# Kernel tuning notes

Hardware: AMD Instinct MI355X
Metric: run time of the kernel (lower is better)

Reference implementation:

```python
import jax, jax.numpy as jnp
import numpy as np
import math

B, S, D, H = 2, 2048, 2048, 16
DH = D // H  # head dim = 128
THETA = 10000.0


def _rope(x, pos):
    """Interleaved RoPE. x: [..., S, DH], pos: [S] (int)."""
    dh = x.shape[-1]
    freqs = (1.0 / THETA) ** (2.0 * jnp.arange(dh // 2, dtype=jnp.float32) / dh)  # [DH/2]
    ang = pos.astype(jnp.float32)[:, None] * freqs[None, :]  # [S, DH/2]
    cos = jnp.cos(ang).astype(x.dtype)
    sin = jnp.sin(ang).astype(x.dtype)
    xe = x[..., 0::2]
    xo = x[..., 1::2]
    oe = xe * cos - xo * sin
    oo = xe * sin + xo * cos
    return jnp.stack([oe, oo], axis=-1).reshape(x.shape)


def setup_inputs() -> dict:
    key = jax.random.key(0)
    ks = jax.random.split(key, 5)
    std = 2.0 / math.sqrt(D + D)
    x = jax.random.normal(ks[0], (B, S, D), dtype=jnp.float32)
    Wq = jax.random.normal(ks[1], (D, D), dtype=jnp.float32) * std
    Wk = jax.random.normal(ks[2], (D, D), dtype=jnp.float32) * std
    Wv = jax.random.normal(ks[3], (D, D), dtype=jnp.float32) * std
    Wo = jax.random.normal(ks[4], (D, D), dtype=jnp.float32) * std
    token_positions = jnp.arange(S, dtype=jnp.int64 if jax.config.jax_enable_x64 else jnp.int32)[None, :]
    return {"x": x, "token_positions": token_positions, "Wq": Wq, "Wk": Wk, "Wv": Wv, "Wo": Wo}


def reference(x, token_positions, Wq, Wk, Wv, Wo):
    b, s, d = x.shape
    pos = token_positions[0]  # [S]
    # QKV projections (Linear is x @ W.T, no bias)
    Q = (x @ Wq.T).reshape(b, s, H, DH).transpose(0, 2, 1, 3)  # [b,h,s,dh]
    K = (x @ Wk.T).reshape(b, s, H, DH).transpose(0, 2, 1, 3)
    V = (x @ Wv.T).reshape(b, s, H, DH).transpose(0, 2, 1, 3)
    # per-head RoPE on Q and K
    Q = _rope(Q, pos)
    K = _rope(K, pos)
    # scaled dot-product attention with causal mask
    scores = jnp.einsum('bhqd,bhkd->bhqk', Q, K) / math.sqrt(DH)
    causal = jnp.tril(jnp.ones((s, s), dtype=bool))  # [s,s]
    scores = jnp.where(causal[None, None, :, :], scores, -jnp.inf)
    prob = jax.nn.softmax(scores, axis=-1)
    O = jnp.einsum('bhqk,bhkd->bhqd', prob, V)  # [b,h,s,dh]
    O = O.transpose(0, 2, 1, 3).reshape(b, s, d)
    return O @ Wo.T
```

## Files before the change

kernel.cpp:

```cpp
#include <hip/hip_runtime.h>
#include <hip/hip_bf16.h>
#include <math.h>

#define BB 2
#define SS 2048
#define DD 2048
#define HH 16
#define DHH 128
#define MM (BB*SS)

typedef __attribute__((ext_vector_type(8))) short bf16x8;
typedef __attribute__((ext_vector_type(4))) float f32x4;

#define AS1 __attribute__((address_space(1)))
#define AS3 __attribute__((address_space(3)))
#define GLOAD_LDS16(g, l) __builtin_amdgcn_global_load_lds((const AS1 void*)(g), (AS3 void*)(l), 16, 0, 0)

#if __has_builtin(__builtin_amdgcn_exp2f)
#define EXP2F(x) __builtin_amdgcn_exp2f(x)
#else
#define EXP2F(x) exp2f(x)
#endif

__device__ __forceinline__ float b2f(short s) {
  union { unsigned int u; float f; } v;
  v.u = ((unsigned int)(unsigned short)s) << 16;
  return v.f;
}
__device__ __forceinline__ short f2b(float f) {
  union { float f; unsigned int u; } v; v.f = f;
  unsigned int u = v.u;
  u += 0x7fffu + ((u >> 16) & 1u);
  return (short)(u >> 16);
}
__device__ __forceinline__ short f2b_fast(float f) {
  union { float f; unsigned int u; } v; v.f = f;
  return (short)((v.u + 0x8000u) >> 16);
}

template<int CTRL>
__device__ __forceinline__ float dppf(float x) {
  int xi = __builtin_bit_cast(int, x);
  int r = __builtin_amdgcn_update_dpp(0, xi, CTRL, 0xf, 0xf, true);
  return __builtin_bit_cast(float, r);
}
__device__ __forceinline__ float rmax16(float x) {
  x = fmaxf(x, dppf<0xB1>(x));
  x = fmaxf(x, dppf<0x4E>(x));
  x = fmaxf(x, dppf<0x141>(x));
  x = fmaxf(x, dppf<0x140>(x));
  return x;
}
__device__ __forceinline__ float rsum16(float x) {
  x += dppf<0xB1>(x);
  x += dppf<0x4E>(x);
  x += dppf<0x141>(x);
  x += dppf<0x140>(x);
  return x;
}

__global__ void cvt_all(const float* __restrict__ x,  const float* __restrict__ wq,
                        const float* __restrict__ wk, const float* __restrict__ wv,
                        const float* __restrict__ wo,
                        short* __restrict__ xb,  short* __restrict__ wqb,
                        short* __restrict__ wkb, short* __restrict__ wvb,
                        short* __restrict__ wob) {
  int i = blockIdx.x * blockDim.x + threadIdx.x;
  const float* src; short* dst; int off;
  if (i < 2097152) { src = x; dst = xb; off = i; }
  else {
    int j = i - 2097152;
    int w = j >> 20; off = j & 1048575;
    src = (w == 0) ? wq : (w == 1) ? wk : (w == 2) ? wv : wo;
    dst = (w == 0) ? wqb : (w == 1) ? wkb : (w == 2) ? wvb : wob;
  }
  float4 v = ((const float4*)src)[i < 2097152 ? off : off];
  short4 o;
  o.x = f2b(v.x); o.y = f2b(v.y); o.z = f2b(v.z); o.w = f2b(v.w);
  ((short4*)dst)[off] = o;
}

#define LDA3(b, mt, kk) (*(const bf16x8*)((const char*)smA + (b)*32768 + \
    (wm*64 + (mt)*16 + l16)*128 + ((((kk)*64) + quad*16) ^ ((l16 & 7) << 4))))
#define LDB3(b, nt, kk) (*(const bf16x8*)((const char*)smB + (b)*16384 + \
    (wn*64 + (nt)*16 + l16)*128 + ((((kk)*64) + quad*16) ^ ((l16 & 7) << 4))))
#define STGA4(b, t) do { \
    _Pragma("unroll") \
    for (int h = 0; h < 4; ++h) \
      GLOAD_LDS16(aBase + (size_t)(h*64) * DD + (t)*64, smA + (b)*16384 + h*4096 + wst); } while(0)
#define STGB2M(b, t) do { \
    _Pragma("unroll") \
    for (int h = 0; h < 2; ++h) \
      GLOAD_LDS16(bBase + (size_t)(h*64) * DD + (t)*64, smB + (b)*8192 + h*4096 + wst); } while(0)
#define MFMA_P(NT0) do { \
    __builtin_amdgcn_s_setprio(1); \
    _Pragma("unroll") \
    for (int mt = 0; mt < 4; ++mt) \
      _Pragma("unroll") \
      for (int nt = 0; nt < 2; ++nt) \
        _Pragma("unroll") \
        for (int kk = 0; kk < 2; ++kk) \
          acc[mt][(NT0) + nt] = __builtin_amdgcn_mfma_f32_16x16x32_bf16( \
              af[mt][kk], bf[(NT0) + nt][kk], acc[mt][(NT0) + nt], 0, 0, 0); \
    __builtin_amdgcn_s_setprio(0); } while(0)

#define GEMM_KLOOP \
  STGA4(0, 0); STGB2M(0, 0); \
  STGA4(1, 1); STGB2M(1, 1); \
  asm volatile("s_waitcnt vmcnt(6)" ::: "memory"); \
  __builtin_amdgcn_s_barrier(); \
  int bc = 0, bs = 2; \
  for (int t = 0; t < 32; ++t) { \
    _Pragma("unroll") \
    for (int mt = 0; mt < 4; ++mt) { af[mt][0] = LDA3(bc, mt, 0); af[mt][1] = LDA3(bc, mt, 1); } \
    _Pragma("unroll") \
    for (int nt = 0; nt < 2; ++nt) { bf[nt][0] = LDB3(bc, nt, 0); bf[nt][1] = LDB3(bc, nt, 1); } \
    if (t + 2 < 32) STGA4(bs, t + 2); \
    __builtin_amdgcn_s_barrier(); \
    asm volatile("s_waitcnt lgkmcnt(0)" ::: "memory"); \
    __builtin_amdgcn_sched_barrier(0); \
    MFMA_P(0); \
    __builtin_amdgcn_s_barrier(); \
    _Pragma("unroll") \
    for (int nt = 2; nt < 4; ++nt) { bf[nt][0] = LDB3(bc, nt, 0); bf[nt][1] = LDB3(bc, nt, 1); } \
    if (t + 2 < 32) { \
      STGB2M(bs, t + 2); \
      asm volatile("s_waitcnt vmcnt(6)" ::: "memory"); \
    } else { \
      asm volatile("s_waitcnt vmcnt(0)" ::: "memory"); \
    } \
    __builtin_amdgcn_s_barrier(); \
    asm volatile("s_waitcnt lgkmcnt(0)" ::: "memory"); \
    __builtin_amdgcn_sched_barrier(0); \
    MFMA_P(2); \
    __builtin_amdgcn_s_barrier(); \
    bc = (bc == 2) ? 0 : bc + 1; \
    bs = (bs == 2) ? 0 : bs + 1; \
  }

__global__ __launch_bounds__(512, 1)
void gemm_qkv(const short* __restrict__ A,
              const short* __restrict__ Wq, const short* __restrict__ Wk,
              const short* __restrict__ Wv, const int* __restrict__ pos,
              short* __restrict__ Qo, short* __restrict__ Ko, short* __restrict__ Vo) {
  __shared__ __align__(16) short sm[73728];
  const int tid = threadIdx.x;
  const int lane = tid & 63;
  const int wave = tid >> 6;
  const int quad = lane >> 4, l16 = lane & 15;
  const int wm = wave >> 1, wn = wave & 1;

  const int wid = (blockIdx.x & 7) * 96 + (blockIdx.x >> 3);
  const int wsel = wid >> 8;
  const int idr = wid & 255;
  const int bm = (idr >> 4) * 256;
  const int bn = (idr & 15) * 128;
  const short* Bw = (wsel == 0) ? Wq : (wsel == 1) ? Wk : Wv;
  short* Cout = (wsel == 0) ? Qo : (wsel == 1) ? Ko : Vo;

  short* smA = sm;
  short* smB = sm + 49152;
  const int wst = wave * 512;

  const int srow = tid >> 3;
  const int scol = ((tid & 7) ^ (srow & 7)) * 8;
  const short* aBase = A  + (size_t)(bm + srow) * DD + scol;
  const short* bBase = Bw + (size_t)(bn + srow) * DD + scol;

  f32x4 acc[4][4] = {};
  bf16x8 af[4][2], bf[4][2];

  GEMM_KLOOP

  if (wsel < 2) {
    const float post = (wsel == 0) ? 0.1275174306f : 1.0f;
    float fr[4];
    #pragma unroll
    for (int nt = 0; nt < 4; ++nt) {
      int pi = wn * 32 + nt * 8 + (l16 >> 1);
      fr[nt] = __expf(-0.14391156831f * (float)pi);
    }
    const float sgn = (l16 & 1) ? 1.0f : -1.0f;
    #pragma unroll
    for (int mt = 0; mt < 4; ++mt) {
      #pragma unroll
      for (int r = 0; r < 4; ++r) {
        int m = bm + wm*64 + mt*16 + quad*4 + r;
        float fp = (float)pos[m & 2047];
        #pragma unroll
        for (int nt = 0; nt < 4; ++nt) {
          float v = acc[mt][nt][r];
          float p = dppf<0xB1>(v);
          float ang = fp * fr[nt];
          float sn = __sinf(ang), cs = __cosf(ang);
          acc[mt][nt][r] = (v * cs + sgn * p * sn) * post;
        }
      }
    }
  }

  #pragma unroll
  for (int mt = 0; mt < 4; ++mt)
    #pragma unroll
    for (int nt = 0; nt < 4; ++nt)
      #pragma unroll
      for (int r = 0; r < 4; ++r) {
        int m = bm + wm*64 + mt*16 + quad*4 + r;
        int n = bn + wn*64 + nt*16 + l16;
        int b = m >> 11, s = m & 2047;
        int h = n >> 7,  d = n & 127;
        Cout[(((size_t)(b*HH + h)*SS + s)*DHH) + d] = f2b(acc[mt][nt][r]);
      }
}

__global__ __launch_bounds__(512, 1)
void gemm_o(const short* __restrict__ A, const short* __restrict__ Bw,
            float* __restrict__ Cout) {
  __shared__ __align__(16) short sm[73728];
  const int tid = threadIdx.x;
  const int lane = tid & 63;
  const int wave = tid >> 6;
  const int quad = lane >> 4, l16 = lane & 15;
  const int wm = wave >> 1, wn = wave & 1;

  const int wid = (blockIdx.x & 7) * 32 + (blockIdx.x >> 3);
  const int bm = (wid >> 4) * 256;
  const int bn = (wid & 15) * 128;

  short* smA = sm;
  short* smB = sm + 49152;
  const int wst = wave * 512;

  const int srow = tid >> 3;
  const int scol = ((tid & 7) ^ (srow & 7)) * 8;
  const short* aBase = A  + (size_t)(bm + srow) * DD + scol;
  const short* bBase = Bw + (size_t)(bn + srow) * DD + scol;

  f32x4 acc[4][4] = {};
  bf16x8 af[4][2], bf[4][2];

  GEMM_KLOOP

  #pragma unroll
  for (int mt = 0; mt < 4; ++mt)
    #pragma unroll
    for (int nt = 0; nt < 4; ++nt)
      #pragma unroll
      for (int r = 0; r < 4; ++r) {
        int m = bm + wm*64 + mt*16 + quad*4 + r;
        int n = bn + wn*64 + nt*16 + l16;
        Cout[(size_t)m * DD + n] = acc[mt][nt][r];
      }
}

__global__ __launch_bounds__(256, 3)
void attn(const short* __restrict__ Q, const short* __restrict__ K,
          const short* __restrict__ V, short* __restrict__ O) {
  __shared__ __align__(16) short Ks[64*128];
  __shared__ __align__(16) short Vt[128*64];
  __shared__ __align__(16) short Pb[4*16*64];
  const int tid = threadIdx.x;
  const int lane = tid & 63, wave = tid >> 6;
  const int quad = lane >> 4, l16 = lane & 15;
  const int L = blockIdx.x;
  const int bh = L & 31;
  const int s = L >> 5;
  const int qt = (s < 8) ? 31 - s : (s < 16) ? s - 8 : (s < 24) ? 39 - s : s - 16;
  const int b = bh >> 4, h = bh & 15;
  const short* Kg = K + (size_t)bh * SS * DHH;
  const short* Vg = V + (size_t)bh * SS * DHH;
  const int qbase = qt * 64 + wave * 16;

  bf16x8 aq[4];
  {
    const short* qp = Q + ((size_t)bh * SS + qbase + l16) * DHH + quad*8;
    #pragma unroll
    for (int ks = 0; ks < 4; ++ks) aq[ks] = *(const bf16x8*)(qp + ks*32);
  }

  f32x4 o[8] = {};
  float mrow[4], lrow[4];
  #pragma unroll
  for (int r = 0; r < 4; ++r) { mrow[r] = -1e30f; lrow[r] = 0.f; }

  const int skey0 = wave*16 + (lane >> 4);
  const int scolb = (lane & 15) << 4;
  const int vkp = (tid & 31) * 2;
  const int vds = (tid >> 5) * 16;

  const int nkt = qt + 1;
  int4 vreg[4];
  {
    const short* vp = Vg + (size_t)vkp * DHH + vds;
    vreg[0] = *(const int4*)vp;         vreg[1] = *(const int4*)(vp + 8);
    vreg[2] = *(const int4*)(vp + DHH); vreg[3] = *(const int4*)(vp + DHH + 8);
  }

  for (int kt = 0; kt < nkt; ++kt) {
    {
      const short* Kt = Kg + (size_t)kt * 64 * DHH;
      #pragma unroll
      for (int j = 0; j < 4; ++j) {
        int key = skey0 + j*4;
        GLOAD_LDS16(Kt + (size_t)key * DHH + ((scolb ^ ((key & 7) << 4)) >> 1),
                    Ks + wave*2048 + j*512);
      }
    }
    asm volatile("" ::: "memory");
    {
      const short* s0 = (const short*)&vreg[0];
      const short* s1 = (const short*)&vreg[2];
      #pragma unroll
      for (int e = 0; e < 16; ++e) {
        int dim = vds + e;
        int val = (int)(unsigned short)s0[e] | ((int)(unsigned short)s1[e] << 16);
        *(int*)((char*)Vt + dim*128 + ((vkp*2) ^ ((dim & 7) << 4))) = val;
      }
    }
    if (kt + 1 < nkt) {
      const short* vp = Vg + (size_t)((kt+1)*64 + vkp) * DHH + vds;
      vreg[0] = *(const int4*)vp;         vreg[1] = *(const int4*)(vp + 8);
      vreg[2] = *(const int4*)(vp + DHH); vreg[3] = *(const int4*)(vp + DHH + 8);
      asm volatile("s_waitcnt vmcnt(4) lgkmcnt(0)" ::: "memory");
    } else {
      asm volatile("s_waitcnt vmcnt(0) lgkmcnt(0)" ::: "memory");
    }
    __builtin_amdgcn_s_barrier();
    __builtin_amdgcn_sched_barrier(0);

    float sv[4][4];
    __builtin_amdgcn_s_setprio(1);
    #pragma unroll
    for (int nt = 0; nt < 4; ++nt) {
      f32x4 a = {0.f, 0.f, 0.f, 0.f};
      #pragma unroll
      for (int ks = 0; ks < 4; ++ks) {
        int key = nt*16 + l16;
        bf16x8 bk = *(const bf16x8*)((const char*)Ks + key*256 +
                       ((ks*64 + quad*16) ^ ((key & 7) << 4)));
        a = __builtin_amdgcn_mfma_f32_16x16x32_bf16(aq[ks], bk, a, 0, 0, 0);
      }
      #pragma unroll
      for (int r = 0; r < 4; ++r) sv[nt][r] = a[r];
    }
    __builtin_amdgcn_s_setprio(0);

    if (kt == qt) {
      #pragma unroll
      for (int nt = 0; nt < 4; ++nt)
        #pragma unroll
        for (int r = 0; r < 4; ++r)
          if (nt*16 + l16 > wave*16 + quad*4 + r) sv[nt][r] = -1e30f;
    }

    #pragma unroll
    for (int r = 0; r < 4; ++r) {
      float mx = fmaxf(fmaxf(sv[0][r], sv[1][r]), fmaxf(sv[2][r], sv[3][r]));
      mx = rmax16(mx);
      float mnew = fmaxf(mrow[r], mx);
      float alpha = EXP2F(mrow[r] - mnew);
      float ls = 0.f;
      #pragma unroll
      for (int nt = 0; nt < 4; ++nt) {
        float pv = EXP2F(sv[nt][r] - mnew);
        sv[nt][r] = pv; ls += pv;
      }
      ls = rsum16(ls);
      lrow[r] = lrow[r] * alpha + ls;
      mrow[r] = mnew;
      #pragma unroll
      for (int nt = 0; nt < 8; ++nt) o[nt][r] *= alpha;
    }

    #pragma unroll
    for (int nt = 0; nt < 4; ++nt)
      #pragma unroll
      for (int r = 0; r < 4; ++r) {
        int qr = quad*4 + r;
        *(short*)((char*)Pb + wave*2048 + qr*128 +
                  (((nt*16 + l16)*2) ^ ((qr & 7) << 4))) = f2b_fast(sv[nt][r]);
      }

    bf16x8 ap[2];
    #pragma unroll
    for (int k2 = 0; k2 < 2; ++k2)
      ap[k2] = *(const bf16x8*)((const char*)Pb + wave*2048 + l16*128 +
                  ((k2*64 + quad*16) ^ ((l16 & 7) << 4)));

    __builtin_amdgcn_s_setprio(1);
    #pragma unroll
    for (int k2 = 0; k2 < 2; ++k2)
      #pragma unroll
      for (int nt = 0; nt < 8; ++nt) {
        int d = nt*16 + l16;
        bf16x8 bv = *(const bf16x8*)((const char*)Vt + d*128 +
                       ((k2*64 + quad*16) ^ ((d & 7) << 4)));
        o[nt] = __builtin_amdgcn_mfma_f32_16x16x32_bf16(ap[k2], bv, o[nt], 0, 0, 0);
      }
    __builtin_amdgcn_s_setprio(0);

    asm volatile("s_waitcnt lgkmcnt(0)" ::: "memory");
    __builtin_amdgcn_s_barrier();
    __builtin_amdgcn_sched_barrier(0);
  }

  #pragma unroll
  for (int nt = 0; nt < 8; ++nt)
    #pragma unroll
    for (int r = 0; r < 4; ++r) {
      int q = qbase + quad*4 + r;
      float v = o[nt][r] / lrow[r];
      O[((size_t)(b*SS + q)) * DD + h*DHH + nt*16 + l16] = f2b(v);
    }
}

extern "C" void kernel_launch(void* const* d_in, const int* in_sizes, int n_in,
                              void* d_out, int out_size, void* d_ws, size_t ws_size,
                              hipStream_t stream) {
  const float* x  = (const float*)d_in[0];
  const int* pos  = (const int*)d_in[1];
  const float* Wq = (const float*)d_in[2];
  const float* Wk = (const float*)d_in[3];
  const float* Wv = (const float*)d_in[4];
  const float* Wo = (const float*)d_in[5];

  char* ws = (char*)d_ws;
  short* xb  = (short*)(ws);
  short* wqb = (short*)(ws + 16777216);
  short* wkb = (short*)(ws + 25165824);
  short* wvb = (short*)(ws + 33554432);
  short* wob = (short*)(ws + 41943040);
  short* Qb  = (short*)(ws + 50331648);
  short* Kb  = (short*)(ws + 67108864);
  short* Vb  = (short*)(ws + 83886080);
  short* Ob  = (short*)(ws + 100663296);

  cvt_all<<<24576, 256, 0, stream>>>(x, Wq, Wk, Wv, Wo, xb, wqb, wkb, wvb, wob);

  gemm_qkv<<<768, 512, 0, stream>>>(xb, wqb, wkb, wvb, pos, Qb, Kb, Vb);

  attn<<<1024, 256, 0, stream>>>(Qb, Kb, Vb, Ob);

  gemm_o<<<256, 512, 0, stream>>>(Ob, wob, (float*)d_out);
}
```

Baseline: 379.7 us.

## Enlarge QKV GEMM tile to 256x256 with quadrant-staged double buffering

Rewrites the QKV projection GEMM to use 256x256 output tiles per 512-thread block instead of 256x128, which halves the grid to 384 blocks and doubles each wave's accumulator footprint. The K loop becomes double-buffered and split into four quadrant MFMA phases, with global-to-LDS loads of the next tiles interleaved between them. The aim is higher arithmetic intensity and fewer redundant operand loads. The cost is more register pressure and fewer blocks to spread across CUs, which can leave the last wave of blocks unevenly balanced. The RoPE epilogue and output indexing are remapped to the new tile layout.

```diff
diff --git a/kernel.cpp b/kernel.cpp
--- a/kernel.cpp
+++ b/kernel.cpp
@@ -80,6 +80,147 @@
   ((short4*)dst)[off] = o;
 }
 
+#define QLDA(cb, mtq, mt, kk) (*(const bf16x8*)((const char*)smA + (cb)*32768 + \
+    ((mtq)*128 + wm*64 + (mt)*16 + l16)*128 + ((((kk)*64) + quad*16) ^ ((l16 & 7) << 4))))
+#define QLDB(cb, ntq, nt, kk) (*(const bf16x8*)((const char*)smB + (cb)*32768 + \
+    ((ntq)*128 + wn*32 + (nt)*16 + l16)*128 + ((((kk)*64) + quad*16) ^ ((l16 & 7) << 4))))
+#define QSTGA(b, t, h) do { \
+    GLOAD_LDS16(aBase + (size_t)((h)*128) * DD + (t)*64,      smA_s + (b)*16384 + ((h)*128)*64 + wst); \
+    GLOAD_LDS16(aBase + (size_t)((h)*128 + 64) * DD + (t)*64, smA_s + (b)*16384 + ((h)*128 + 64)*64 + wst); } while(0)
+#define QSTGB(b, t, h) do { \
+    GLOAD_LDS16(bBase + (size_t)((h)*128) * DD + (t)*64,      smB_s + (b)*16384 + ((h)*128)*64 + wst); \
+    GLOAD_LDS16(bBase + (size_t)((h)*128 + 64) * DD + (t)*64, smB_s + (b)*16384 + ((h)*128 + 64)*64 + wst); } while(0)
+#define QMFMA(MTQ, NTQ) do { \
+    __builtin_amdgcn_s_setprio(1); \
+    _Pragma("unroll") \
+    for (int mt = 0; mt < 4; ++mt) \
+      _Pragma("unroll") \
+      for (int nt = 0; nt < 2; ++nt) \
+        _Pragma("unroll") \
+        for (int kk = 0; kk < 2; ++kk) \
+          acc[(MTQ)*4 + mt][(NTQ)*2 + nt] = __builtin_amdgcn_mfma_f32_16x16x32_bf16( \
+              af[mt][kk], bf[(NTQ)*2 + nt][kk], acc[(MTQ)*4 + mt][(NTQ)*2 + nt], 0, 0, 0); \
+    __builtin_amdgcn_s_setprio(0); } while(0)
+
+__global__ __launch_bounds__(512, 1)
+void gemm_qkv(const short* __restrict__ A,
+              const short* __restrict__ Wq, const short* __restrict__ Wk,
+              const short* __restrict__ Wv, const int* __restrict__ pos,
+              short* __restrict__ Qo, short* __restrict__ Ko, short* __restrict__ Vo) {
+  __shared__ __align__(16) short sm[65536];
+  const int tid = threadIdx.x;
+  const int lane = tid & 63;
+  const int wave = tid >> 6;
+  const int quad = lane >> 4, l16 = lane & 15;
+  const int wm = wave >> 2, wn = wave & 3;
+
+  const int wid = (blockIdx.x & 7) * 48 + (blockIdx.x >> 3);
+  const int wsel = wid >> 7;
+  const int idr = wid & 127;
+  const int bm = (idr >> 3) * 256;
+  const int bn = (idr & 7) * 256;
+  const short* Bw = (wsel == 0) ? Wq : (wsel == 1) ? Wk : Wv;
+  short* Cout = (wsel == 0) ? Qo : (wsel == 1) ? Ko : Vo;
+
+  short* smA_s = sm;
+  short* smB_s = sm + 32768;
+  const char* smA = (const char*)sm;
+  const char* smB = (const char*)(sm + 32768);
+  const int wst = wave * 512;
+
+  const int srow = tid >> 3;
+  const int scol = ((tid & 7) ^ (srow & 7)) * 8;
+  const short* aBase = A  + (size_t)(bm + srow) * DD + scol;
+  const short* bBase = Bw + (size_t)(bn + srow) * DD + scol;
+
+  f32x4 acc[8][4] = {};
+  bf16x8 af[4][2], bf[4][2];
+
+  QSTGA(0, 0, 0); QSTGB(0, 0, 0); QSTGB(0, 0, 1);
+  QSTGA(0, 0, 1); QSTGA(1, 1, 0); QSTGB(1, 1, 1);
+  asm volatile("s_waitcnt vmcnt(6)" ::: "memory");
+  __builtin_amdgcn_s_barrier();
+
+  for (int t = 0; t < 32; ++t) {
+    const int cb = t & 1, nb = cb ^ 1;
+    #pragma unroll
+    for (int mt = 0; mt < 4; ++mt) { af[mt][0] = QLDA(cb, 0, mt, 0); af[mt][1] = QLDA(cb, 0, mt, 1); }
+    #pragma unroll
+    for (int nt = 0; nt < 2; ++nt) { bf[nt][0] = QLDB(cb, 0, nt, 0); bf[nt][1] = QLDB(cb, 0, nt, 1); }
+    if (t + 1 < 32) QSTGB(nb, t + 1, 0);
+    asm volatile("s_waitcnt lgkmcnt(8)" ::: "memory");
+    __builtin_amdgcn_s_barrier();
+    asm volatile("s_waitcnt lgkmcnt(0)" ::: "memory");
+    QMFMA(0, 0);
+    __builtin_amdgcn_s_barrier();
+    #pragma unroll
+    for (int nt = 0; nt < 2; ++nt) { bf[2+nt][0] = QLDB(cb, 1, nt, 0); bf[2+nt][1] = QLDB(cb, 1, nt, 1); }
+    if (t + 1 < 32) QSTGA(nb, t + 1, 1);
+    if (t + 2 < 32) asm volatile("s_waitcnt vmcnt(6)" ::: "memory");
+    else            asm volatile("s_waitcnt vmcnt(0)" ::: "memory");
+    __builtin_amdgcn_s_barrier();
+    asm volatile("s_waitcnt lgkmcnt(0)" ::: "memory");
+    QMFMA(0, 1);
+    __builtin_amdgcn_s_barrier();
+    #pragma unroll
+    for (int mt = 0; mt < 4; ++mt) { af[mt][0] = QLDA(cb, 1, mt, 0); af[mt][1] = QLDA(cb, 1, mt, 1); }
+    if (t + 2 < 32) QSTGA(cb, t + 2, 0);
+    __builtin_amdgcn_s_barrier();
+    asm volatile("s_waitcnt lgkmcnt(0)" ::: "memory");
+    QMFMA(1, 1);
+    __builtin_amdgcn_s_barrier();
+    if (t + 2 < 32) {
+      QSTGB(cb, t + 2, 1);
+      asm volatile("s_waitcnt vmcnt(6)" ::: "memory");
+    } else {
+      asm volatile("s_waitcnt vmcnt(0)" ::: "memory");
+    }
+    __builtin_amdgcn_s_barrier();
+    QMFMA(1, 0);
+    __builtin_amdgcn_s_barrier();
+  }
+
+  if (wsel < 2) {
+    const float post = (wsel == 0) ? 0.1275174306f : 1.0f;
+    float fr[2];
+    #pragma unroll
+    for (int ntl = 0; ntl < 2; ++ntl) {
+      int pi = wn * 16 + ntl * 8 + (l16 >> 1);
+      fr[ntl] = __expf(-0.14391156831f * (float)pi);
+    }
+    const float sgn = (l16 & 1) ? 1.0f : -1.0f;
+    #pragma unroll
+    for (int MT = 0; MT < 8; ++MT) {
+      #pragma unroll
+      for (int r = 0; r < 4; ++r) {
+        int m = bm + (MT >> 2)*128 + wm*64 + (MT & 3)*16 + quad*4 + r;
+        float fp = (float)pos[m & 2047];
+        #pragma unroll
+        for (int NT = 0; NT < 4; ++NT) {
+          float v = acc[MT][NT][r];
+          float p = dppf<0xB1>(v);
+          float ang = fp * fr[NT & 1];
+          float sn = __sinf(ang), cs = __cosf(ang);
+          acc[MT][NT][r] = (v * cs + sgn * p * sn) * post;
+        }
+      }
+    }
+  }
+
+  #pragma unroll
+  for (int MT = 0; MT < 8; ++MT)
+    #pragma unroll
+    for (int NT = 0; NT < 4; ++NT)
+      #pragma unroll
+      for (int r = 0; r < 4; ++r) {
+        int m = bm + (MT >> 2)*128 + wm*64 + (MT & 3)*16 + quad*4 + r;
+        int n = bn + (NT >> 1)*128 + wn*32 + (NT & 1)*16 + l16;
+        int b = m >> 11, s = m & 2047;
+        int h = n >> 7,  d = n & 127;
+        Cout[(((size_t)(b*HH + h)*SS + s)*DHH) + d] = f2b(acc[MT][NT][r]);
+      }
+}
+
 #define LDA3(b, mt, kk) (*(const bf16x8*)((const char*)smA + (b)*32768 + \
     (wm*64 + (mt)*16 + l16)*128 + ((((kk)*64) + quad*16) ^ ((l16 & 7) << 4))))
 #define LDB3(b, nt, kk) (*(const bf16x8*)((const char*)smB + (b)*16384 + \
@@ -137,81 +278,6 @@
     bc = (bc == 2) ? 0 : bc + 1; \
     bs = (bs == 2) ? 0 : bs + 1; \
   }
-
-__global__ __launch_bounds__(512, 1)
-void gemm_qkv(const short* __restrict__ A,
-              const short* __restrict__ Wq, const short* __restrict__ Wk,
-              const short* __restrict__ Wv, const int* __restrict__ pos,
-              short* __restrict__ Qo, short* __restrict__ Ko, short* __restrict__ Vo) {
-  __shared__ __align__(16) short sm[73728];
-  const int tid = threadIdx.x;
-  const int lane = tid & 63;
-  const int wave = tid >> 6;
-  const int quad = lane >> 4, l16 = lane & 15;
-  const int wm = wave >> 1, wn = wave & 1;
-
-  const int wid = (blockIdx.x & 7) * 96 + (blockIdx.x >> 3);
-  const int wsel = wid >> 8;
-  const int idr = wid & 255;
-  const int bm = (idr >> 4) * 256;
-  const int bn = (idr & 15) * 128;
-  const short* Bw = (wsel == 0) ? Wq : (wsel == 1) ? Wk : Wv;
-  short* Cout = (wsel == 0) ? Qo : (wsel == 1) ? Ko : Vo;
-
-  short* smA = sm;
-  short* smB = sm + 49152;
-  const int wst = wave * 512;
-
-  const int srow = tid >> 3;
-  const int scol = ((tid & 7) ^ (srow & 7)) * 8;
-  const short* aBase = A  + (size_t)(bm + srow) * DD + scol;
-  const short* bBase = Bw + (size_t)(bn + srow) * DD + scol;
-
-  f32x4 acc[4][4] = {};
-  bf16x8 af[4][2], bf[4][2];
-
-  GEMM_KLOOP
-
-  if (wsel < 2) {
-    const float post = (wsel == 0) ? 0.1275174306f : 1.0f;
-    float fr[4];
-    #pragma unroll
-    for (int nt = 0; nt < 4; ++nt) {
-      int pi = wn * 32 + nt * 8 + (l16 >> 1);
-      fr[nt] = __expf(-0.14391156831f * (float)pi);
-    }
-    const float sgn = (l16 & 1) ? 1.0f : -1.0f;
-    #pragma unroll
-    for (int mt = 0; mt < 4; ++mt) {
-      #pragma unroll
-      for (int r = 0; r < 4; ++r) {
-        int m = bm + wm*64 + mt*16 + quad*4 + r;
-        float fp = (float)pos[m & 2047];
-        #pragma unroll
-        for (int nt = 0; nt < 4; ++nt) {
-          float v = acc[mt][nt][r];
-          float p = dppf<0xB1>(v);
-          float ang = fp * fr[nt];
-          float sn = __sinf(ang), cs = __cosf(ang);
-          acc[mt][nt][r] = (v * cs + sgn * p * sn) * post;
-        }
-      }
-    }
-  }
-
-  #pragma unroll
-  for (int mt = 0; mt < 4; ++mt)
-    #pragma unroll
-    for (int nt = 0; nt < 4; ++nt)
-      #pragma unroll
-      for (int r = 0; r < 4; ++r) {
-        int m = bm + wm*64 + mt*16 + quad*4 + r;
-        int n = bn + wn*64 + nt*16 + l16;
-        int b = m >> 11, s = m & 2047;
-        int h = n >> 7,  d = n & 127;
-        Cout[(((size_t)(b*HH + h)*SS + s)*DHH) + d] = f2b(acc[mt][nt][r]);
-      }
-}
 
 __global__ __launch_bounds__(512, 1)
 void gemm_o(const short* __restrict__ A, const short* __restrict__ Bw,
@@ -437,7 +503,7 @@
 
   cvt_all<<<24576, 256, 0, stream>>>(x, Wq, Wk, Wv, Wo, xb, wqb, wkb, wvb, wob);
 
-  gemm_qkv<<<768, 512, 0, stream>>>(xb, wqb, wkb, wvb, pos, Qb, Kb, Vb);
+  gemm_qkv<<<384, 512, 0, stream>>>(xb, wqb, wkb, wvb, pos, Qb, Kb, Vb);
 
   attn<<<1024, 256, 0, stream>>>(Qb, Kb, Vb, Ob);
 
```

Measured after the change: 378.3 us. About the same (-0.4%).

## Process 128-query tiles per attention block, two 16-row tiles per wave

Applied to the files above, without the earlier changes.

Each attention workgroup now covers 128 query rows instead of 64, with each wave computing two 16-row query sub-tiles that share each K/V tile loaded into LDS. This halves the grid and roughly halves the global K/V traffic and LDS staging per query row. The cost is doubled accumulator registers, with launch bounds lowered from 3 to 2 blocks per SM, and fewer blocks (512) to balance across CUs. Causal masking now covers the last two key tiles.

```diff
diff --git a/kernel.cpp b/kernel.cpp
--- a/kernel.cpp
+++ b/kernel.cpp
@@ -253,42 +253,45 @@
       }
 }
 
-__global__ __launch_bounds__(256, 3)
+__global__ __launch_bounds__(256, 2)
 void attn(const short* __restrict__ Q, const short* __restrict__ K,
           const short* __restrict__ V, short* __restrict__ O) {
   __shared__ __align__(16) short Ks[64*128];
   __shared__ __align__(16) short Vt[128*64];
-  __shared__ __align__(16) short Pb[4*16*64];
+  __shared__ __align__(16) short Pb[4*32*64];
   const int tid = threadIdx.x;
   const int lane = tid & 63, wave = tid >> 6;
   const int quad = lane >> 4, l16 = lane & 15;
   const int L = blockIdx.x;
   const int bh = L & 31;
   const int s = L >> 5;
-  const int qt = (s < 8) ? 31 - s : (s < 16) ? s - 8 : (s < 24) ? 39 - s : s - 16;
+  const int i = (s < 8) ? s : 23 - s;
   const int b = bh >> 4, h = bh & 15;
   const short* Kg = K + (size_t)bh * SS * DHH;
   const short* Vg = V + (size_t)bh * SS * DHH;
-  const int qbase = qt * 64 + wave * 16;
-
-  bf16x8 aq[4];
-  {
-    const short* qp = Q + ((size_t)bh * SS + qbase + l16) * DHH + quad*8;
-    #pragma unroll
-    for (int ks = 0; ks < 4; ++ks) aq[ks] = *(const bf16x8*)(qp + ks*32);
-  }
-
-  f32x4 o[8] = {};
-  float mrow[4], lrow[4];
+  const int qb0 = i * 128 + wave * 32;
+
+  bf16x8 aq[2][4];
   #pragma unroll
-  for (int r = 0; r < 4; ++r) { mrow[r] = -1e30f; lrow[r] = 0.f; }
+  for (int t = 0; t < 2; ++t) {
+    const short* qp = Q + ((size_t)bh * SS + qb0 + t*16 + l16) * DHH + quad*8;
+    #pragma unroll
+    for (int ks = 0; ks < 4; ++ks) aq[t][ks] = *(const bf16x8*)(qp + ks*32);
+  }
+
+  f32x4 o[2][8] = {};
+  float mrow[2][4], lrow[2][4];
+  #pragma unroll
+  for (int t = 0; t < 2; ++t)
+    #pragma unroll
+    for (int r = 0; r < 4; ++r) { mrow[t][r] = -1e30f; lrow[t][r] = 0.f; }
 
   const int skey0 = wave*16 + (lane >> 4);
   const int scolb = (lane & 15) << 4;
   const int vkp = (tid & 31) * 2;
   const int vds = (tid >> 5) * 16;
 
-  const int nkt = qt + 1;
+  const int nkt = 2*i + 2;
   int4 vreg[4];
   {
     const short* vp = Vg + (size_t)vkp * DHH + vds;
@@ -328,64 +331,71 @@
     __builtin_amdgcn_s_barrier();
     __builtin_amdgcn_sched_barrier(0);
 
-    float sv[4][4];
+    float sv[2][4][4];
     __builtin_amdgcn_s_setprio(1);
     #pragma unroll
     for (int nt = 0; nt < 4; ++nt) {
-      f32x4 a = {0.f, 0.f, 0.f, 0.f};
+      f32x4 a0 = {0.f,0.f,0.f,0.f}, a1 = {0.f,0.f,0.f,0.f};
       #pragma unroll
       for (int ks = 0; ks < 4; ++ks) {
         int key = nt*16 + l16;
         bf16x8 bk = *(const bf16x8*)((const char*)Ks + key*256 +
                        ((ks*64 + quad*16) ^ ((key & 7) << 4)));
-        a = __builtin_amdgcn_mfma_f32_16x16x32_bf16(aq[ks], bk, a, 0, 0, 0);
-      }
-      #pragma unroll
-      for (int r = 0; r < 4; ++r) sv[nt][r] = a[r];
+        a0 = __builtin_amdgcn_mfma_f32_16x16x32_bf16(aq[0][ks], bk, a0, 0, 0, 0);
+        a1 = __builtin_amdgcn_mfma_f32_16x16x32_bf16(aq[1][ks], bk, a1, 0, 0, 0);
+      }
+      #pragma unroll
+      for (int r = 0; r < 4; ++r) { sv[0][nt][r] = a0[r]; sv[1][nt][r] = a1[r]; }
     }
     __builtin_amdgcn_s_setprio(0);
 
-    if (kt == qt) {
+    if (kt >= nkt - 2) {
+      #pragma unroll
+      for (int t = 0; t < 2; ++t)
+        #pragma unroll
+        for (int nt = 0; nt < 4; ++nt)
+          #pragma unroll
+          for (int r = 0; r < 4; ++r)
+            if (kt*64 + nt*16 + l16 > qb0 + t*16 + quad*4 + r) sv[t][nt][r] = -1e30f;
+    }
+
+    #pragma unroll
+    for (int t = 0; t < 2; ++t) {
+      #pragma unroll
+      for (int r = 0; r < 4; ++r) {
+        float mx = fmaxf(fmaxf(sv[t][0][r], sv[t][1][r]), fmaxf(sv[t][2][r], sv[t][3][r]));
+        mx = rmax16(mx);
+        float mnew = fmaxf(mrow[t][r], mx);
+        float alpha = EXP2F(mrow[t][r] - mnew);
+        float ls = 0.f;
+        #pragma unroll
+        for (int nt = 0; nt < 4; ++nt) {
+          float pv = EXP2F(sv[t][nt][r] - mnew);
+          sv[t][nt][r] = pv; ls += pv;
+        }
+        ls = rsum16(ls);
+        lrow[t][r] = lrow[t][r] * alpha + ls;
+        mrow[t][r] = mnew;
+        #pragma unroll
+        for (int nt = 0; nt < 8; ++nt) o[t][nt][r] *= alpha;
+      }
       #pragma unroll
       for (int nt = 0; nt < 4; ++nt)
         #pragma unroll
-        for (int r = 0; r < 4; ++r)
-          if (nt*16 + l16 > wave*16 + quad*4 + r) sv[nt][r] = -1e30f;
-    }
-
-    #pragma unroll
-    for (int r = 0; r < 4; ++r) {
-      float mx = fmaxf(fmaxf(sv[0][r], sv[1][r]), fmaxf(sv[2][r], sv[3][r]));
-      mx = rmax16(mx);
-      float mnew = fmaxf(mrow[r], mx);
-      float alpha = EXP2F(mrow[r] - mnew);
-      float ls = 0.f;
-      #pragma unroll
-      for (int nt = 0; nt < 4; ++nt) {
-        float pv = EXP2F(sv[nt][r] - mnew);
-        sv[nt][r] = pv; ls += pv;
-      }
-      ls = rsum16(ls);
-      lrow[r] = lrow[r] * alpha + ls;
-      mrow[r] = mnew;
-      #pragma unroll
-      for (int nt = 0; nt < 8; ++nt) o[nt][r] *= alpha;
-    }
-
-    #pragma unroll
-    for (int nt = 0; nt < 4; ++nt)
-      #pragma unroll
-      for (int r = 0; r < 4; ++r) {
-        int qr = quad*4 + r;
-        *(short*)((char*)Pb + wave*2048 + qr*128 +
-                  (((nt*16 + l16)*2) ^ ((qr & 7) << 4))) = f2b_fast(sv[nt][r]);
-      }
-
-    bf16x8 ap[2];
-    #pragma unroll
-    for (int k2 = 0; k2 < 2; ++k2)
-      ap[k2] = *(const bf16x8*)((const char*)Pb + wave*2048 + l16*128 +
-                  ((k2*64 + quad*16) ^ ((l16 & 7) << 4)));
+        for (int r = 0; r < 4; ++r) {
+          int qr = t*16 + quad*4 + r;
+          *(short*)((char*)Pb + wave*4096 + qr*128 +
+                    (((nt*16 + l16)*2) ^ ((qr & 7) << 4))) = f2b_fast(sv[t][nt][r]);
+        }
+    }
+
+    bf16x8 ap[2][2];
+    #pragma unroll
+    for (int t = 0; t < 2; ++t)
+      #pragma unroll
+      for (int k2 = 0; k2 < 2; ++k2)
+        ap[t][k2] = *(const bf16x8*)((const char*)Pb + wave*4096 + (t*16 + l16)*128 +
+                      ((k2*64 + quad*16) ^ ((l16 & 7) << 4)));
 
     __builtin_amdgcn_s_setprio(1);
     #pragma unroll
@@ -395,7 +405,8 @@
         int d = nt*16 + l16;
         bf16x8 bv = *(const bf16x8*)((const char*)Vt + d*128 +
                        ((k2*64 + quad*16) ^ ((d & 7) << 4)));
-        o[nt] = __builtin_amdgcn_mfma_f32_16x16x32_bf16(ap[k2], bv, o[nt], 0, 0, 0);
+        o[0][nt] = __builtin_amdgcn_mfma_f32_16x16x32_bf16(ap[0][k2], bv, o[0][nt], 0, 0, 0);
+        o[1][nt] = __builtin_amdgcn_mfma_f32_16x16x32_bf16(ap[1][k2], bv, o[1][nt], 0, 0, 0);
       }
     __builtin_amdgcn_s_setprio(0);
 
@@ -405,13 +416,15 @@
   }
 
   #pragma unroll
-  for (int nt = 0; nt < 8; ++nt)
-    #pragma unroll
-    for (int r = 0; r < 4; ++r) {
-      int q = qbase + quad*4 + r;
-      float v = o[nt][r] / lrow[r];
-      O[((size_t)(b*SS + q)) * DD + h*DHH + nt*16 + l16] = f2b(v);
-    }
+  for (int t = 0; t < 2; ++t)
+    #pragma unroll
+    for (int nt = 0; nt < 8; ++nt)
+      #pragma unroll
+      for (int r = 0; r < 4; ++r) {
+        int q = qb0 + t*16 + quad*4 + r;
+        float v = o[t][nt][r] / lrow[t][r];
+        O[((size_t)(b*SS + q)) * DD + h*DHH + nt*16 + l16] = f2b(v);
+      }
 }
 
 extern "C" void kernel_launch(void* const* d_in, const int* in_sizes, int n_in,
@@ -439,7 +452,7 @@
 
   gemm_qkv<<<768, 512, 0, stream>>>(xb, wqb, wkb, wvb, pos, Qb, Kb, Vb);
 
-  attn<<<1024, 256, 0, stream>>>(Qb, Kb, Vb, Ob);
+  attn<<<512, 256, 0, stream>>>(Qb, Kb, Vb, Ob);
 
   gemm_o<<<256, 512, 0, stream>>>(Ob, wob, (float*)d_out);
 }
```

Measured after the change: 380.8 us. About the same (+0.3%).
